# Optimization experiments

Measured on AMD Instinct MI355X. Metric: run time of the kernel, lower is better.

The kernel has to match this reference:

```python
import jax, jax.numpy as jnp
import numpy as np

LEVELS = (16384, 8192, 4096, 2048)  # static 1D spatial shape of each feature level


def setup_inputs() -> dict:
    key = jax.random.key(0)
    k1, k2, k3 = jax.random.split(key, 3)
    bs, H, D = 4, 8, 32
    nq, Lv, P = 4096, len(LEVELS), 8
    num_keys = sum(LEVELS)
    value = jax.random.normal(k1, (bs, num_keys, H, D), dtype=jnp.float32)
    sampling_locations = jax.random.uniform(k2, (bs, nq, H, Lv, P, 1), dtype=jnp.float32)
    sampling_weights = jax.random.uniform(k3, (bs, nq, H, Lv, P), dtype=jnp.float32)
    return {"value": value, "sampling_locations": sampling_locations,
            "sampling_weights": sampling_weights}


def reference(value, sampling_locations, sampling_weights):
    # value: (bs, num_keys, H, D); locations: (bs, nq, H, Lv, P, 1) in [0,1];
    # weights: (bs, nq, H, Lv, P). Output: (bs, nq, H*D), head-major channels.
    bs, _, H, D = value.shape
    nq = sampling_locations.shape[1]
    P = sampling_locations.shape[4]
    offsets = np.concatenate([[0], np.cumsum(LEVELS)])
    sampled = []
    for lvl, L in enumerate(LEVELS):
        v = value[:, offsets[lvl]:offsets[lvl + 1]]              # (bs, L, H, D)
        v = jnp.transpose(v, (0, 2, 1, 3))                       # (bs, H, L, D)
        # grid coordinate: loc * L - 1 (matches sampling_grid_l_ * L_ - 1)
        x = sampling_locations[:, :, :, lvl, :, 0] * L - 1.0     # (bs, nq, H, P)
        x = jnp.transpose(x, (0, 2, 1, 3))                       # (bs, H, nq, P)
        x_low = jnp.floor(x)
        lx = x - x_low                                           # frac weight for high
        hx = 1.0 - lx                                            # frac weight for low
        xl = x_low.astype(jnp.int32)
        xh = xl + 1
        m_low = ((xl >= 0) & (xl < L)).astype(v.dtype)           # zeros padding masks
        m_high = ((xh >= 0) & (xh < L)).astype(v.dtype)
        idx_l = jnp.clip(xl, 0, L - 1).reshape(bs, H, nq * P)
        idx_h = jnp.clip(xh, 0, L - 1).reshape(bs, H, nq * P)
        v1 = jnp.take_along_axis(v, idx_l[..., None], axis=2).reshape(bs, H, nq, P, D)
        v2 = jnp.take_along_axis(v, idx_h[..., None], axis=2).reshape(bs, H, nq, P, D)
        v1 = v1 * m_low[..., None]
        v2 = v2 * m_high[..., None]
        sampled.append(hx[..., None] * v1 + lx[..., None] * v2)  # (bs, H, nq, P, D)
    samp = jnp.stack(sampled, axis=3)                            # (bs, H, nq, Lv, P, D)
    w = jnp.transpose(sampling_weights, (0, 2, 1, 3, 4))         # (bs, H, nq, Lv, P)
    out = jnp.einsum('bhqlpd,bhqlp->bqhd', samp, w)              # weighted sum
    return out.reshape(bs, nq, H * D)
```

## Files before the change

### kernel.cpp

```cpp
#include <hip/hip_runtime.h>
#include <hip/hip_fp16.h>

#define NQ 4096
#define NH 8
#define ND 32
#define NK 30720
#define LDSS 33

__global__ __launch_bounds__(256) void cvt_kernel(const float* __restrict__ v,
                                                  uint4* __restrict__ o, int n8) {
    int i = blockIdx.x * blockDim.x + threadIdx.x;
    const float4* __restrict__ v4 = (const float4*)v;
    for (; i < n8; i += gridDim.x * blockDim.x) {
        const float4 f0 = v4[2 * i];
        const float4 f1 = v4[2 * i + 1];
        __half2 h0 = __floats2half2_rn(f0.x, f0.y);
        __half2 h1 = __floats2half2_rn(f0.z, f0.w);
        __half2 h2 = __floats2half2_rn(f1.x, f1.y);
        __half2 h3 = __floats2half2_rn(f1.z, f1.w);
        uint4 u;
        u.x = *reinterpret_cast<unsigned*>(&h0);
        u.y = *reinterpret_cast<unsigned*>(&h1);
        u.z = *reinterpret_cast<unsigned*>(&h2);
        u.w = *reinterpret_cast<unsigned*>(&h3);
        o[i] = u;
    }
}

template <bool FP16>
__global__ __launch_bounds__(256, 8) void spd_kernel(
    const float* __restrict__ value,
    const __half* __restrict__ vh,
    const float* __restrict__ loc,
    const float* __restrict__ wts,
    float* __restrict__ out)
{
    const int tid = threadIdx.x;
    const int g  = blockIdx.x & 7;
    const int w  = blockIdx.x >> 3;
    const int b  = g >> 1;
    const int hh = g & 1;
    const int q0 = w << 3;

    __shared__ uint2 s_d[32 * LDSS];

    const size_t base = ((size_t)(b * NQ + q0) * 8 + hh * 4) * 32;
    #pragma unroll
    for (int e = 0; e < 4; ++e) {
        const int ent = (e << 8) | tid;
        const size_t gidx = base + (size_t)(ent >> 7) * 256 + (ent & 127);
        const float x_loc = loc[gidx];
        const float wq    = wts[gidx];

        const int l   = (ent >> 3) & 3;
        const int L   = 16384 >> l;
        const int off = 32768 - (32768 >> l);

        const float x  = x_loc * (float)L - 1.0f;
        const float xf = floorf(x);
        const float lx = x - xf;
        const float hx = 1.0f - lx;
        const int   xl = (int)xf;
        const int   xh = xl + 1;

        const bool ok1 = (xl >= 0) && (xl < L);
        const bool ok2 = (xh >= 0) && (xh < L);
        int c1 = xl < 0 ? 0 : (xl > L - 1 ? L - 1 : xl);
        int c2 = xh < 0 ? 0 : (xh > L - 1 ? L - 1 : xh);
        const float w1 = ok1 ? wq * hx : 0.0f;
        const float w2 = ok2 ? wq * lx : 0.0f;

        const int li = (ent & 31) * LDSS + (ent >> 5);
        __half2 wh = __floats2half2_rn(w1, w2);
        uint2 d;
        d.x = (unsigned)(off + c1) | ((unsigned)(off + c2) << 16);
        d.y = *reinterpret_cast<unsigned*>(&wh);
        s_d[li] = d;
    }
    __syncthreads();

    const int qi = tid >> 5;
    const int cb = tid >> 3;
    const int h  = (hh << 2) | ((tid >> 3) & 3);
    const int d4 = tid & 7;
    const unsigned lane = (unsigned)((h << 3) | d4);

    float4 acc = make_float4(0.f, 0.f, 0.f, 0.f);

    if (FP16) {
        const uint2* __restrict__ vb2 =
            (const uint2*)(vh) + (size_t)b * (NK * 64);
        #pragma unroll 16
        for (int j = 0; j < 32; ++j) {
            const uint2 d = s_d[j * LDSS + cb];
            const __half2 wh = *reinterpret_cast<const __half2*>(&d.y);
            const float w1 = __low2float(wh);
            const float w2 = __high2float(wh);
            const uint2 r1 = vb2[((d.x & 0xffffu) << 6) + lane];
            const uint2 r2 = vb2[((d.x >> 16) << 6) + lane];
            const float2 a0 = __half22float2(*(const __half2*)&r1.x);
            const float2 a1 = __half22float2(*(const __half2*)&r1.y);
            const float2 c0 = __half22float2(*(const __half2*)&r2.x);
            const float2 c1 = __half22float2(*(const __half2*)&r2.y);
            acc.x += w1 * a0.x + w2 * c0.x;
            acc.y += w1 * a0.y + w2 * c0.y;
            acc.z += w1 * a1.x + w2 * c1.x;
            acc.w += w1 * a1.y + w2 * c1.y;
        }
    } else {
        const float4* __restrict__ vb4 =
            (const float4*)(value) + (size_t)b * (NK * 64);
        #pragma unroll 16
        for (int j = 0; j < 32; ++j) {
            const uint2 d = s_d[j * LDSS + cb];
            const __half2 wh = *reinterpret_cast<const __half2*>(&d.y);
            const float w1 = __low2float(wh);
            const float w2 = __high2float(wh);
            const float4 a = vb4[(size_t)((d.x & 0xffffu) << 6) + lane];
            const float4 c = vb4[(size_t)((d.x >> 16) << 6) + lane];
            acc.x += w1 * a.x + w2 * c.x;
            acc.y += w1 * a.y + w2 * c.y;
            acc.z += w1 * a.z + w2 * c.z;
            acc.w += w1 * a.w + w2 * c.w;
        }
    }

    float4* __restrict__ o4 = (float4*)out;
    o4[(size_t)(b * NQ + q0 + qi) * 64 + lane] = acc;
}

extern "C" void kernel_launch(void* const* d_in, const int* in_sizes, int n_in,
                              void* d_out, int out_size, void* d_ws, size_t ws_size,
                              hipStream_t stream) {
    const float* value = (const float*)d_in[0];
    const float* loc   = (const float*)d_in[1];
    const float* wts   = (const float*)d_in[2];
    float* out = (float*)d_out;

    const int bs = 4;
    const int blocks = 8 * (NQ / 8);
    const size_t need = (size_t)bs * NK * NH * ND * sizeof(__half);

    if (ws_size >= need) {
        const int n8 = bs * NK * NH * ND / 8;
        cvt_kernel<<<2048, 256, 0, stream>>>(value, (uint4*)d_ws, n8);
        spd_kernel<true><<<blocks, 256, 0, stream>>>(value, (const __half*)d_ws,
                                                     loc, wts, out);
    } else {
        spd_kernel<false><<<blocks, 256, 0, stream>>>(value, nullptr,
                                                      loc, wts, out);
    }
}
```

Baseline: 82.29 us.

## Process 16 queries per block with 8 channels per thread

Each block now handles 16 queries instead of 8, and each thread accumulates 8 output channels using 16-byte fp16 gathers instead of 4 channels with 8-byte gathers. This halves the block count and widens each memory access, with the aim of reducing per-block setup overhead and the number of gather instructions. The cost is more registers per thread (the occupancy hint drops from 8 to 6), a larger LDS table, and less parallelism to hide gather latency.

```diff
diff --git a/kernel.cpp b/kernel.cpp
--- a/kernel.cpp
+++ b/kernel.cpp
@@ -5,7 +5,7 @@
 #define NH 8
 #define ND 32
 #define NK 30720
-#define LDSS 33
+#define LDSS 65
 
 __global__ __launch_bounds__(256) void cvt_kernel(const float* __restrict__ v,
                                                   uint4* __restrict__ o, int n8) {
@@ -28,7 +28,7 @@
 }
 
 template <bool FP16>
-__global__ __launch_bounds__(256, 8) void spd_kernel(
+__global__ __launch_bounds__(256, 6) void spd_kernel(
     const float* __restrict__ value,
     const __half* __restrict__ vh,
     const float* __restrict__ loc,
@@ -40,13 +40,13 @@
     const int w  = blockIdx.x >> 3;
     const int b  = g >> 1;
     const int hh = g & 1;
-    const int q0 = w << 3;
+    const int q0 = w << 4;
 
     __shared__ uint2 s_d[32 * LDSS];
 
     const size_t base = ((size_t)(b * NQ + q0) * 8 + hh * 4) * 32;
     #pragma unroll
-    for (int e = 0; e < 4; ++e) {
+    for (int e = 0; e < 8; ++e) {
         const int ent = (e << 8) | tid;
         const size_t gidx = base + (size_t)(ent >> 7) * 256 + (ent & 127);
         const float x_loc = loc[gidx];
@@ -79,54 +79,75 @@
     }
     __syncthreads();
 
-    const int qi = tid >> 5;
-    const int cb = tid >> 3;
-    const int h  = (hh << 2) | ((tid >> 3) & 3);
-    const int d4 = tid & 7;
-    const unsigned lane = (unsigned)((h << 3) | d4);
+    const int qi = tid >> 4;
+    const int cb = tid >> 2;
+    const int h4 = (tid >> 2) & 3;
+    const int d2 = tid & 3;
+    const int h  = (hh << 2) | h4;
 
-    float4 acc = make_float4(0.f, 0.f, 0.f, 0.f);
+    float acc[8] = {0.f, 0.f, 0.f, 0.f, 0.f, 0.f, 0.f, 0.f};
 
     if (FP16) {
-        const uint2* __restrict__ vb2 =
-            (const uint2*)(vh) + (size_t)b * (NK * 64);
-        #pragma unroll 16
+        const uint4* __restrict__ vbu =
+            (const uint4*)(vh) + (size_t)b * (NK * 32);
+        const unsigned lane4 = (unsigned)((h << 2) | d2);
+        #pragma unroll 8
         for (int j = 0; j < 32; ++j) {
             const uint2 d = s_d[j * LDSS + cb];
             const __half2 wh = *reinterpret_cast<const __half2*>(&d.y);
             const float w1 = __low2float(wh);
             const float w2 = __high2float(wh);
-            const uint2 r1 = vb2[((d.x & 0xffffu) << 6) + lane];
-            const uint2 r2 = vb2[((d.x >> 16) << 6) + lane];
+            const uint4 r1 = vbu[((d.x & 0xffffu) << 5) + lane4];
+            const uint4 r2 = vbu[((d.x >> 16) << 5) + lane4];
             const float2 a0 = __half22float2(*(const __half2*)&r1.x);
             const float2 a1 = __half22float2(*(const __half2*)&r1.y);
+            const float2 a2 = __half22float2(*(const __half2*)&r1.z);
+            const float2 a3 = __half22float2(*(const __half2*)&r1.w);
             const float2 c0 = __half22float2(*(const __half2*)&r2.x);
             const float2 c1 = __half22float2(*(const __half2*)&r2.y);
-            acc.x += w1 * a0.x + w2 * c0.x;
-            acc.y += w1 * a0.y + w2 * c0.y;
-            acc.z += w1 * a1.x + w2 * c1.x;
-            acc.w += w1 * a1.y + w2 * c1.y;
+            const float2 c2 = __half22float2(*(const __half2*)&r2.z);
+            const float2 c3 = __half22float2(*(const __half2*)&r2.w);
+            acc[0] += w1 * a0.x + w2 * c0.x;
+            acc[1] += w1 * a0.y + w2 * c0.y;
+            acc[2] += w1 * a1.x + w2 * c1.x;
+            acc[3] += w1 * a1.y + w2 * c1.y;
+            acc[4] += w1 * a2.x + w2 * c2.x;
+            acc[5] += w1 * a2.y + w2 * c2.y;
+            acc[6] += w1 * a3.x + w2 * c3.x;
+            acc[7] += w1 * a3.y + w2 * c3.y;
         }
     } else {
         const float4* __restrict__ vb4 =
             (const float4*)(value) + (size_t)b * (NK * 64);
-        #pragma unroll 16
+        const unsigned lf = (unsigned)((h << 3) | (d2 << 1));
+        #pragma unroll 8
         for (int j = 0; j < 32; ++j) {
             const uint2 d = s_d[j * LDSS + cb];
             const __half2 wh = *reinterpret_cast<const __half2*>(&d.y);
             const float w1 = __low2float(wh);
             const float w2 = __high2float(wh);
-            const float4 a = vb4[(size_t)((d.x & 0xffffu) << 6) + lane];
-            const float4 c = vb4[(size_t)((d.x >> 16) << 6) + lane];
-            acc.x += w1 * a.x + w2 * c.x;
-            acc.y += w1 * a.y + w2 * c.y;
-            acc.z += w1 * a.z + w2 * c.z;
-            acc.w += w1 * a.w + w2 * c.w;
+            const unsigned k1 = (d.x & 0xffffu) << 6;
+            const unsigned k2 = (d.x >> 16) << 6;
+            const float4 a0 = vb4[k1 + lf];
+            const float4 a1 = vb4[k1 + lf + 1];
+            const float4 c0 = vb4[k2 + lf];
+            const float4 c1 = vb4[k2 + lf + 1];
+            acc[0] += w1 * a0.x + w2 * c0.x;
+            acc[1] += w1 * a0.y + w2 * c0.y;
+            acc[2] += w1 * a0.z + w2 * c0.z;
+            acc[3] += w1 * a0.w + w2 * c0.w;
+            acc[4] += w1 * a1.x + w2 * c1.x;
+            acc[5] += w1 * a1.y + w2 * c1.y;
+            acc[6] += w1 * a1.z + w2 * c1.z;
+            acc[7] += w1 * a1.w + w2 * c1.w;
         }
     }
 
     float4* __restrict__ o4 = (float4*)out;
-    o4[(size_t)(b * NQ + q0 + qi) * 64 + lane] = acc;
+    const size_t orow = (size_t)(b * NQ + q0 + qi) * 64;
+    const unsigned oc = (unsigned)((h << 3) | (d2 << 1));
+    o4[orow + oc]     = make_float4(acc[0], acc[1], acc[2], acc[3]);
+    o4[orow + oc + 1] = make_float4(acc[4], acc[5], acc[6], acc[7]);
 }
 
 extern "C" void kernel_launch(void* const* d_in, const int* in_sizes, int n_in,
@@ -138,7 +159,7 @@
     float* out = (float*)d_out;
 
     const int bs = 4;
-    const int blocks = 8 * (NQ / 8);
+    const int blocks = 8 * (NQ / 16);
     const size_t need = (size_t)bs * NK * NH * ND * sizeof(__half);
 
     if (ws_size >= need) {
```

Result: slower. 84.05 us (+2.1%).

## Split sampling kernel into level-0 pass and accumulating pass over remaining levels

Applied to the files above, without the earlier changes.

Splits the fused sampling kernel into two launches. The first processes only the largest level (rows 0-7) and writes the output. The second processes levels 1-3 and accumulates onto the output it reads back. The likely aim is better cache locality, since each pass gathers from a smaller slice of the value tensor. In exchange it adds a kernel launch, an extra read and write of the output, and a second load of the location and weight metadata.

```diff
diff --git a/kernel.cpp b/kernel.cpp
--- a/kernel.cpp
+++ b/kernel.cpp
@@ -27,7 +27,7 @@
     }
 }
 
-template <bool FP16>
+template <int J0, int J1, bool ACCUM, bool FP16>
 __global__ __launch_bounds__(256, 8) void spd_kernel(
     const float* __restrict__ value,
     const __half* __restrict__ vh,
@@ -35,24 +35,27 @@
     const float* __restrict__ wts,
     float* __restrict__ out)
 {
+    constexpr int NROWS = J1 - J0;
     const int tid = threadIdx.x;
-    const int g  = blockIdx.x & 7;
+    const int g8 = blockIdx.x & 7;
     const int w  = blockIdx.x >> 3;
-    const int b  = g >> 1;
-    const int hh = g & 1;
+    const int b  = g8 >> 1;
+    const int hh = g8 & 1;
     const int q0 = w << 3;
 
-    __shared__ uint2 s_d[32 * LDSS];
+    __shared__ uint2 s_d[NROWS * LDSS];
 
-    const size_t base = ((size_t)(b * NQ + q0) * 8 + hh * 4) * 32;
+    const size_t base = (size_t)(b * NQ + q0) * 256 + hh * 128;
     #pragma unroll
-    for (int e = 0; e < 4; ++e) {
-        const int ent = (e << 8) | tid;
-        const size_t gidx = base + (size_t)(ent >> 7) * 256 + (ent & 127);
+    for (int e = 0; e < (NROWS * 32) / 256; ++e) {
+        const int idx = (e << 8) | tid;
+        const int row = J0 + (idx >> 5);
+        const int col = idx & 31;
+        const size_t gidx = base + (size_t)(col >> 2) * 256 + ((col & 3) << 5) + row;
         const float x_loc = loc[gidx];
         const float wq    = wts[gidx];
 
-        const int l   = (ent >> 3) & 3;
+        const int l   = row >> 3;
         const int L   = 16384 >> l;
         const int off = 32768 - (32768 >> l);
 
@@ -70,28 +73,29 @@
         const float w1 = ok1 ? wq * hx : 0.0f;
         const float w2 = ok2 ? wq * lx : 0.0f;
 
-        const int li = (ent & 31) * LDSS + (ent >> 5);
         __half2 wh = __floats2half2_rn(w1, w2);
         uint2 d;
         d.x = (unsigned)(off + c1) | ((unsigned)(off + c2) << 16);
         d.y = *reinterpret_cast<unsigned*>(&wh);
-        s_d[li] = d;
+        s_d[(row - J0) * LDSS + col] = d;
     }
     __syncthreads();
 
-    const int qi = tid >> 5;
     const int cb = tid >> 3;
     const int h  = (hh << 2) | ((tid >> 3) & 3);
     const int d4 = tid & 7;
     const unsigned lane = (unsigned)((h << 3) | d4);
+    float4* __restrict__ o4 = (float4*)out;
+    const size_t oidx = (size_t)(b * NQ + q0 + (tid >> 5)) * 64 + lane;
 
     float4 acc = make_float4(0.f, 0.f, 0.f, 0.f);
+    if (ACCUM) acc = o4[oidx];
 
     if (FP16) {
         const uint2* __restrict__ vb2 =
             (const uint2*)(vh) + (size_t)b * (NK * 64);
-        #pragma unroll 16
-        for (int j = 0; j < 32; ++j) {
+        #pragma unroll 8
+        for (int j = 0; j < NROWS; ++j) {
             const uint2 d = s_d[j * LDSS + cb];
             const __half2 wh = *reinterpret_cast<const __half2*>(&d.y);
             const float w1 = __low2float(wh);
@@ -110,8 +114,8 @@
     } else {
         const float4* __restrict__ vb4 =
             (const float4*)(value) + (size_t)b * (NK * 64);
-        #pragma unroll 16
-        for (int j = 0; j < 32; ++j) {
+        #pragma unroll 8
+        for (int j = 0; j < NROWS; ++j) {
             const uint2 d = s_d[j * LDSS + cb];
             const __half2 wh = *reinterpret_cast<const __half2*>(&d.y);
             const float w1 = __low2float(wh);
@@ -125,8 +129,7 @@
         }
     }
 
-    float4* __restrict__ o4 = (float4*)out;
-    o4[(size_t)(b * NQ + q0 + qi) * 64 + lane] = acc;
+    o4[oidx] = acc;
 }
 
 extern "C" void kernel_launch(void* const* d_in, const int* in_sizes, int n_in,
@@ -144,10 +147,12 @@
     if (ws_size >= need) {
         const int n8 = bs * NK * NH * ND / 8;
         cvt_kernel<<<2048, 256, 0, stream>>>(value, (uint4*)d_ws, n8);
-        spd_kernel<true><<<blocks, 256, 0, stream>>>(value, (const __half*)d_ws,
-                                                     loc, wts, out);
+        spd_kernel<0, 8, false, true><<<blocks, 256, 0, stream>>>(
+            value, (const __half*)d_ws, loc, wts, out);
+        spd_kernel<8, 32, true, true><<<blocks, 256, 0, stream>>>(
+            value, (const __half*)d_ws, loc, wts, out);
     } else {
-        spd_kernel<false><<<blocks, 256, 0, stream>>>(value, nullptr,
-                                                      loc, wts, out);
+        spd_kernel<0, 32, false, false><<<blocks, 256, 0, stream>>>(
+            value, nullptr, loc, wts, out);
     }
 }
```

Measured after the change: 104.1 us. 26.5% more time.

## Transpose fp16 value to head-major layout and fetch both bilinear taps per load

Applied to the files above, without the earlier changes.

The conversion kernel now writes the fp16 copy of value in (batch, head, key, dim) order, so two adjacent keys for one head sit next to each other in memory. The sampling kernel stores a single base index per sample and has eight lanes read a contiguous 128-byte span covering both neighbouring keys. Each lane applies either the low or high weight, and the halves are combined with a cross-lane shuffle. This replaces two scattered gathers per sample with one contiguous load, at the cost of a strided transpose write and extra shuffle work. Edge handling is reworked so the xl==-1 case puts its weight on key 0.

```diff
diff --git a/kernel.cpp b/kernel.cpp
--- a/kernel.cpp
+++ b/kernel.cpp
@@ -7,24 +7,27 @@
 #define NK 30720
 #define LDSS 33
 
-__global__ __launch_bounds__(256) void cvt_kernel(const float* __restrict__ v,
-                                                  uint4* __restrict__ o, int n8) {
-    int i = blockIdx.x * blockDim.x + threadIdx.x;
+__global__ __launch_bounds__(256) void cvt_t_kernel(const float* __restrict__ v,
+                                                    uint4* __restrict__ o) {
+    const int bh = blockIdx.x / 480;
+    const int kc = blockIdx.x - bh * 480;
+    const int b  = bh >> 3, h = bh & 7;
+    const int chunk = (kc << 8) | threadIdx.x;
+    const int key = chunk >> 2, qt = chunk & 3;
     const float4* __restrict__ v4 = (const float4*)v;
-    for (; i < n8; i += gridDim.x * blockDim.x) {
-        const float4 f0 = v4[2 * i];
-        const float4 f1 = v4[2 * i + 1];
-        __half2 h0 = __floats2half2_rn(f0.x, f0.y);
-        __half2 h1 = __floats2half2_rn(f0.z, f0.w);
-        __half2 h2 = __floats2half2_rn(f1.x, f1.y);
-        __half2 h3 = __floats2half2_rn(f1.z, f1.w);
-        uint4 u;
-        u.x = *reinterpret_cast<unsigned*>(&h0);
-        u.y = *reinterpret_cast<unsigned*>(&h1);
-        u.z = *reinterpret_cast<unsigned*>(&h2);
-        u.w = *reinterpret_cast<unsigned*>(&h3);
-        o[i] = u;
-    }
+    const size_t ii = ((size_t)(b * NK + key) * 8 + h) * 8 + qt * 2;
+    const float4 f0 = v4[ii];
+    const float4 f1 = v4[ii + 1];
+    __half2 h0 = __floats2half2_rn(f0.x, f0.y);
+    __half2 h1 = __floats2half2_rn(f0.z, f0.w);
+    __half2 h2 = __floats2half2_rn(f1.x, f1.y);
+    __half2 h3 = __floats2half2_rn(f1.z, f1.w);
+    uint4 u;
+    u.x = *reinterpret_cast<unsigned*>(&h0);
+    u.y = *reinterpret_cast<unsigned*>(&h1);
+    u.z = *reinterpret_cast<unsigned*>(&h2);
+    u.w = *reinterpret_cast<unsigned*>(&h3);
+    o[(size_t)bh * (NK * 4) + chunk] = u;
 }
 
 template <bool FP16>
@@ -36,10 +39,10 @@
     float* __restrict__ out)
 {
     const int tid = threadIdx.x;
-    const int g  = blockIdx.x & 7;
+    const int g8 = blockIdx.x & 7;
     const int w  = blockIdx.x >> 3;
-    const int b  = g >> 1;
-    const int hh = g & 1;
+    const int b  = g8 >> 1;
+    const int hh = g8 & 1;
     const int q0 = w << 3;
 
     __shared__ uint2 s_d[32 * LDSS];
@@ -61,72 +64,83 @@
         const float lx = x - xf;
         const float hx = 1.0f - lx;
         const int   xl = (int)xf;
-        const int   xh = xl + 1;
 
-        const bool ok1 = (xl >= 0) && (xl < L);
-        const bool ok2 = (xh >= 0) && (xh < L);
-        int c1 = xl < 0 ? 0 : (xl > L - 1 ? L - 1 : xl);
-        int c2 = xh < 0 ? 0 : (xh > L - 1 ? L - 1 : xh);
-        const float w1 = ok1 ? wq * hx : 0.0f;
-        const float w2 = ok2 ? wq * lx : 0.0f;
+        int   bse = 0;
+        float wa = 0.0f, wb = 0.0f;
+        if (xl >= 0 && xl < L) {
+            bse = xl;
+            wa  = wq * hx;
+            wb  = (xl + 1 < L) ? wq * lx : 0.0f;
+        } else if (xl == -1) {
+            bse = 0;
+            wa  = wq * lx;
+            wb  = 0.0f;
+        }
 
         const int li = (ent & 31) * LDSS + (ent >> 5);
-        __half2 wh = __floats2half2_rn(w1, w2);
+        __half2 wh = __floats2half2_rn(wa, wb);
         uint2 d;
-        d.x = (unsigned)(off + c1) | ((unsigned)(off + c2) << 16);
+        d.x = (unsigned)(off + bse);
         d.y = *reinterpret_cast<unsigned*>(&wh);
         s_d[li] = d;
     }
     __syncthreads();
 
-    const int qi = tid >> 5;
     const int cb = tid >> 3;
+    const int ls = tid & 7;
     const int h  = (hh << 2) | ((tid >> 3) & 3);
-    const int d4 = tid & 7;
-    const unsigned lane = (unsigned)((h << 3) | d4);
 
-    float4 acc = make_float4(0.f, 0.f, 0.f, 0.f);
+    float acc[8] = {0.f, 0.f, 0.f, 0.f, 0.f, 0.f, 0.f, 0.f};
 
     if (FP16) {
-        const uint2* __restrict__ vb2 =
-            (const uint2*)(vh) + (size_t)b * (NK * 64);
-        #pragma unroll 16
+        const uint4* __restrict__ vb =
+            (const uint4*)vh + (size_t)((b << 3) | h) * (NK * 4);
+        #pragma unroll 8
         for (int j = 0; j < 32; ++j) {
             const uint2 d = s_d[j * LDSS + cb];
             const __half2 wh = *reinterpret_cast<const __half2*>(&d.y);
-            const float w1 = __low2float(wh);
-            const float w2 = __high2float(wh);
-            const uint2 r1 = vb2[((d.x & 0xffffu) << 6) + lane];
-            const uint2 r2 = vb2[((d.x >> 16) << 6) + lane];
-            const float2 a0 = __half22float2(*(const __half2*)&r1.x);
-            const float2 a1 = __half22float2(*(const __half2*)&r1.y);
-            const float2 c0 = __half22float2(*(const __half2*)&r2.x);
-            const float2 c1 = __half22float2(*(const __half2*)&r2.y);
-            acc.x += w1 * a0.x + w2 * c0.x;
-            acc.y += w1 * a0.y + w2 * c0.y;
-            acc.z += w1 * a1.x + w2 * c1.x;
-            acc.w += w1 * a1.y + w2 * c1.y;
+            const float myw = (ls < 4) ? __low2float(wh) : __high2float(wh);
+            const uint4 r = vb[(d.x << 2) + ls];
+            const float2 v0 = __half22float2(*(const __half2*)&r.x);
+            const float2 v1 = __half22float2(*(const __half2*)&r.y);
+            const float2 v2 = __half22float2(*(const __half2*)&r.z);
+            const float2 v3 = __half22float2(*(const __half2*)&r.w);
+            acc[0] += myw * v0.x;  acc[1] += myw * v0.y;
+            acc[2] += myw * v1.x;  acc[3] += myw * v1.y;
+            acc[4] += myw * v2.x;  acc[5] += myw * v2.y;
+            acc[6] += myw * v3.x;  acc[7] += myw * v3.y;
+        }
+        #pragma unroll
+        for (int i = 0; i < 8; ++i)
+            acc[i] += __shfl_xor(acc[i], 4, 64);
+        if (ls < 4) {
+            float4* __restrict__ o4 = (float4*)out;
+            const size_t orow = (size_t)(b * NQ + q0 + (cb >> 2)) * 64;
+            o4[orow + (h << 3) + ls * 2]     = make_float4(acc[0], acc[1], acc[2], acc[3]);
+            o4[orow + (h << 3) + ls * 2 + 1] = make_float4(acc[4], acc[5], acc[6], acc[7]);
         }
     } else {
-        const float4* __restrict__ vb4 =
-            (const float4*)(value) + (size_t)b * (NK * 64);
-        #pragma unroll 16
+        const float4* __restrict__ vb4 = (const float4*)value;
+        #pragma unroll 8
         for (int j = 0; j < 32; ++j) {
             const uint2 d = s_d[j * LDSS + cb];
             const __half2 wh = *reinterpret_cast<const __half2*>(&d.y);
-            const float w1 = __low2float(wh);
-            const float w2 = __high2float(wh);
-            const float4 a = vb4[(size_t)((d.x & 0xffffu) << 6) + lane];
-            const float4 c = vb4[(size_t)((d.x >> 16) << 6) + lane];
-            acc.x += w1 * a.x + w2 * c.x;
-            acc.y += w1 * a.y + w2 * c.y;
-            acc.z += w1 * a.z + w2 * c.z;
-            acc.w += w1 * a.w + w2 * c.w;
+            const float wa = __low2float(wh);
+            const float wb = __high2float(wh);
+            const unsigned k2 = (d.x + 1 < NK) ? d.x + 1 : NK - 1;
+            const size_t i1 = ((size_t)(b * NK) + d.x) * 64 + (h << 3) + ls;
+            const size_t i2 = ((size_t)(b * NK) + k2)  * 64 + (h << 3) + ls;
+            const float4 a = vb4[i1];
+            const float4 c = vb4[i2];
+            acc[0] += wa * a.x + wb * c.x;
+            acc[1] += wa * a.y + wb * c.y;
+            acc[2] += wa * a.z + wb * c.z;
+            acc[3] += wa * a.w + wb * c.w;
         }
+        float4* __restrict__ o4 = (float4*)out;
+        o4[(size_t)(b * NQ + q0 + (cb >> 2)) * 64 + (h << 3) + ls] =
+            make_float4(acc[0], acc[1], acc[2], acc[3]);
     }
-
-    float4* __restrict__ o4 = (float4*)out;
-    o4[(size_t)(b * NQ + q0 + qi) * 64 + lane] = acc;
 }
 
 extern "C" void kernel_launch(void* const* d_in, const int* in_sizes, int n_in,
@@ -139,11 +153,10 @@
 
     const int bs = 4;
     const int blocks = 8 * (NQ / 8);
-    const size_t need = (size_t)bs * NK * NH * ND * sizeof(__half);
+    const size_t need = (size_t)bs * NK * NH * ND * sizeof(__half) + 64;
 
     if (ws_size >= need) {
-        const int n8 = bs * NK * NH * ND / 8;
-        cvt_kernel<<<2048, 256, 0, stream>>>(value, (uint4*)d_ws, n8);
+        cvt_t_kernel<<<bs * NH * 480, 256, 0, stream>>>(value, (uint4*)d_ws);
         spd_kernel<true><<<blocks, 256, 0, stream>>>(value, (const __half*)d_ws,
                                                      loc, wts, out);
     } else {
```

New measurement: 91.67 us. 1.11x slower.
